# Kernel tuning notes

Measured on AMD Instinct MI355X. Metric: run time of the kernel, lower is better.

Reference implementation:

```python
import jax, jax.numpy as jnp
import numpy as np

N = 12288      # nodes
F = 512        # input feature dim
H1 = 256       # encoder hidden 1
H2 = 128       # latent dim
E = 393216     # edges (avg degree 32)


def setup_inputs() -> dict:
    key = jax.random.key(0)
    ks = jax.random.split(key, 7)
    x = jax.random.normal(ks[0], (N, F), dtype=jnp.float32)
    src = jax.random.randint(ks[1], (E,), 0, N, dtype=jnp.int64)
    dst = jax.random.randint(ks[2], (E,), 0, N, dtype=jnp.int64)
    # normalized-adjacency-like positive edge values
    edge_val = jax.random.uniform(ks[3], (E,), dtype=jnp.float32) / 32.0
    # xavier-uniform-ish scaled weights
    W1 = jax.random.normal(ks[4], (F, H1), dtype=jnp.float32) * np.float32(np.sqrt(2.0 / (F + H1)))
    W2 = jax.random.normal(ks[5], (H1, H2), dtype=jnp.float32) * np.float32(np.sqrt(2.0 / (H1 + H2)))
    W3 = jax.random.normal(ks[6], (H1, H2), dtype=jnp.float32) * np.float32(np.sqrt(2.0 / (H1 + H2)))
    return {"x": x, "src": src, "dst": dst, "edge_val": edge_val,
            "W1": W1, "W2": W2, "W3": W3}


def _spmm(src, dst, val, dense):
    # out[i] = sum_{e: src[e]==i} val[e] * dense[dst[e]]  -- sparse [N,N] @ dense [N,D]
    msg = val[:, None] * dense[dst]              # [E, D]
    return jax.ops.segment_sum(msg, src, num_segments=N)


def _gcn(h, src, dst, val, W):
    support = h @ W                               # dense GEMM
    return _spmm(src, dst, val, support)


def reference(x, src, dst, edge_val, W1, W2, W3):
    # EncoderCora (eval mode: dropout=0)
    h1 = jax.nn.relu(_gcn(x, src, dst, edge_val, W1))   # [N, H1]
    mu = _gcn(h1, src, dst, edge_val, W2)               # [N, H2]
    logvar = _gcn(h1, src, dst, edge_val, W3)           # [N, H2]
    # reparameterize: eval -> z = mu
    z = mu
    # DecoderCora: inner product + sigmoid
    adj_recon = jax.nn.sigmoid(z @ z.T)                 # [N, N]
    return adj_recon, mu, logvar
```

## Files before the change

### kernel.cpp

```cpp
#include <hip/hip_runtime.h>
#include <stdint.h>


#define NN 12288
#define FF 512
#define HD1 256
#define HD2 128
#define EE 393216

typedef short bf16x8 __attribute__((ext_vector_type(8)));
typedef float f32x16 __attribute__((ext_vector_type(16)));

__device__ inline unsigned short f2b(float f) {
  unsigned int u = __float_as_uint(f);
  unsigned int r = u + 0x7fffu + ((u >> 16) & 1u);
  return (unsigned short)(r >> 16);
}

__device__ inline bf16x8 ldb8(const unsigned short* p) {
  return *(const bf16x8*)p;
}

__device__ inline bf16x8 ldf8(const float* p) {
  float4 v0 = ((const float4*)p)[0];
  float4 v1 = ((const float4*)p)[1];
  bf16x8 r;
  r[0] = (short)f2b(v0.x); r[1] = (short)f2b(v0.y);
  r[2] = (short)f2b(v0.z); r[3] = (short)f2b(v0.w);
  r[4] = (short)f2b(v1.x); r[5] = (short)f2b(v1.y);
  r[6] = (short)f2b(v1.z); r[7] = (short)f2b(v1.w);
  return r;
}

__device__ inline f32x16 mfma32(bf16x8 a, bf16x8 b, f32x16 c) {
  return __builtin_amdgcn_mfma_f32_32x32x16_bf16(a, b, c, 0, 0, 0);
}


__global__ void k_hist(const int* __restrict__ src, int* __restrict__ deg) {
  int e = blockIdx.x * 256 + threadIdx.x;
  atomicAdd(&deg[src[e]], 1);
}

__global__ void k_scan(const int* __restrict__ deg, int* __restrict__ off,
                       int* __restrict__ cur) {
  __shared__ int sdata[256];
  __shared__ int sbase;
  if (threadIdx.x == 0) sbase = 0;
  __syncthreads();
  for (int c = 0; c < NN; c += 256) {
    int v = deg[c + threadIdx.x];
    sdata[threadIdx.x] = v;
    __syncthreads();
    for (int s = 1; s < 256; s <<= 1) {
      int t = (threadIdx.x >= s) ? sdata[threadIdx.x - s] : 0;
      __syncthreads();
      sdata[threadIdx.x] += t;
      __syncthreads();
    }
    int o = sbase + sdata[threadIdx.x] - v;
    off[c + threadIdx.x] = o;
    cur[c + threadIdx.x] = o;
    __syncthreads();
    if (threadIdx.x == 255) sbase += sdata[255];
    __syncthreads();
  }
}

__global__ void k_fill(const int* __restrict__ src, const int* __restrict__ dst,
                       const float* __restrict__ ev, int* __restrict__ cur,
                       int* __restrict__ dstp, float* __restrict__ valp) {
  int e = blockIdx.x * 256 + threadIdx.x;
  int p = atomicAdd(&cur[src[e]], 1);
  dstp[p] = dst[e];
  valp[p] = ev[e];
}


__global__ void k_f2b4(const float* __restrict__ in, unsigned short* __restrict__ outb) {
  int i = blockIdx.x * 256 + threadIdx.x;
  float4 v = ((const float4*)in)[i];
  ushort4 o;
  o.x = f2b(v.x); o.y = f2b(v.y); o.z = f2b(v.z); o.w = f2b(v.w);
  ((ushort4*)outb)[i] = o;
}

__global__ void k_transw(const float* __restrict__ W, unsigned short* __restrict__ Wt,
                         int K, int Ncols) {
  int idx = blockIdx.x * 256 + threadIdx.x;
  if (idx < K * Ncols) {
    int k = idx / Ncols;
    int n = idx - k * Ncols;
    Wt[(size_t)n * K + k] = f2b(W[idx]);
  }
}


__global__ __launch_bounds__(256) void gemm_bt(
    const unsigned short* __restrict__ A, const unsigned short* __restrict__ Bt,
    float* __restrict__ C, int Nn, int K) {
  int wave = threadIdx.x >> 6, lane = threadIdx.x & 63;
  int wr = wave >> 1, wc = wave & 1;
  int row0 = blockIdx.x * 128 + wr * 64;
  int col0 = blockIdx.y * 128 + wc * 64;
  int lm = lane & 31, lk = (lane >> 5) * 8;

  f32x16 acc[2][2] = {};
  const unsigned short* a0p = A + (size_t)(row0 + lm) * K + lk;
  const unsigned short* a1p = a0p + (size_t)32 * K;
  const unsigned short* b0p = Bt + (size_t)(col0 + lm) * K + lk;
  const unsigned short* b1p = b0p + (size_t)32 * K;

  for (int k0 = 0; k0 < K; k0 += 16) {
    bf16x8 a0 = ldb8(a0p + k0), a1 = ldb8(a1p + k0);
    bf16x8 b0 = ldb8(b0p + k0), b1 = ldb8(b1p + k0);
    acc[0][0] = mfma32(a0, b0, acc[0][0]);
    acc[0][1] = mfma32(a0, b1, acc[0][1]);
    acc[1][0] = mfma32(a1, b0, acc[1][0]);
    acc[1][1] = mfma32(a1, b1, acc[1][1]);
  }

#pragma unroll
  for (int ti = 0; ti < 2; ++ti)
#pragma unroll
    for (int tj = 0; tj < 2; ++tj)
#pragma unroll
      for (int r = 0; r < 16; ++r) {
        int row = row0 + ti * 32 + (r & 3) + 8 * (r >> 2) + 4 * (lane >> 5);
        int col = col0 + tj * 32 + lm;
        C[(size_t)row * Nn + col] = acc[ti][tj][r];
      }
}


__global__ __launch_bounds__(256) void k_spmm_relu(
    const int* __restrict__ off, const int* __restrict__ dstp,
    const float* __restrict__ valp, const float* __restrict__ dense,
    unsigned short* __restrict__ outb) {
  int node = blockIdx.x * 4 + (threadIdx.x >> 6);
  int lane = threadIdx.x & 63;
  int e0 = off[node];
  int e1 = (node == NN - 1) ? EE : off[node + 1];
  const float4* dp = (const float4*)dense;
  float4 acc = make_float4(0.f, 0.f, 0.f, 0.f);
  for (int eb = e0; eb < e1; eb += 32) {
    int rem = e1 - eb; if (rem > 32) rem = 32;
    int dd = 0; float vv = 0.f;
    if (lane < rem) { dd = dstp[eb + lane]; vv = valp[eb + lane]; }
    for (int j = 0; j < rem; ++j) {
      int dj = __shfl(dd, j);
      float vj = __shfl(vv, j);
      float4 r = dp[(size_t)dj * 64 + lane];
      acc.x = fmaf(vj, r.x, acc.x);
      acc.y = fmaf(vj, r.y, acc.y);
      acc.z = fmaf(vj, r.z, acc.z);
      acc.w = fmaf(vj, r.w, acc.w);
    }
  }
  ushort4 ob;
  ob.x = f2b(fmaxf(acc.x, 0.f));
  ob.y = f2b(fmaxf(acc.y, 0.f));
  ob.z = f2b(fmaxf(acc.z, 0.f));
  ob.w = f2b(fmaxf(acc.w, 0.f));
  ((ushort4*)outb)[(size_t)node * 64 + lane] = ob;
}

__global__ __launch_bounds__(256) void k_spmm_mlv(
    const int* __restrict__ off, const int* __restrict__ dstp,
    const float* __restrict__ valp, const float* __restrict__ dense,
    float* __restrict__ mu, float* __restrict__ logvar) {
  int node = blockIdx.x * 4 + (threadIdx.x >> 6);
  int lane = threadIdx.x & 63;
  int e0 = off[node];
  int e1 = (node == NN - 1) ? EE : off[node + 1];
  const float4* dp = (const float4*)dense;
  float4 acc = make_float4(0.f, 0.f, 0.f, 0.f);
  for (int eb = e0; eb < e1; eb += 32) {
    int rem = e1 - eb; if (rem > 32) rem = 32;
    int dd = 0; float vv = 0.f;
    if (lane < rem) { dd = dstp[eb + lane]; vv = valp[eb + lane]; }
    for (int j = 0; j < rem; ++j) {
      int dj = __shfl(dd, j);
      float vj = __shfl(vv, j);
      float4 r = dp[(size_t)dj * 64 + lane];
      acc.x = fmaf(vj, r.x, acc.x);
      acc.y = fmaf(vj, r.y, acc.y);
      acc.z = fmaf(vj, r.z, acc.z);
      acc.w = fmaf(vj, r.w, acc.w);
    }
  }
  if (lane < 32) ((float4*)mu)[(size_t)node * 32 + lane] = acc;
  else           ((float4*)logvar)[(size_t)node * 32 + (lane - 32)] = acc;
}


__global__ __launch_bounds__(256) void k_decoder_b(const unsigned short* __restrict__ Zb,
                                                   float* __restrict__ out) {
  int wave = threadIdx.x >> 6, lane = threadIdx.x & 63;
  int wr = wave >> 1, wc = wave & 1;
  int row0 = blockIdx.x * 128 + wr * 64;
  int col0 = blockIdx.y * 128 + wc * 64;
  int lm = lane & 31, lk = (lane >> 5) * 8;

  f32x16 acc[2][2] = {};
  const unsigned short* a0p = Zb + (size_t)(row0 + lm) * HD2 + lk;
  const unsigned short* a1p = a0p + (size_t)32 * HD2;
  const unsigned short* b0p = Zb + (size_t)(col0 + lm) * HD2 + lk;
  const unsigned short* b1p = b0p + (size_t)32 * HD2;

#pragma unroll
  for (int k0 = 0; k0 < HD2; k0 += 16) {
    bf16x8 a0 = ldb8(a0p + k0), a1 = ldb8(a1p + k0);
    bf16x8 b0 = ldb8(b0p + k0), b1 = ldb8(b1p + k0);
    acc[0][0] = mfma32(a0, b0, acc[0][0]);
    acc[0][1] = mfma32(a0, b1, acc[0][1]);
    acc[1][0] = mfma32(a1, b0, acc[1][0]);
    acc[1][1] = mfma32(a1, b1, acc[1][1]);
  }

#pragma unroll
  for (int ti = 0; ti < 2; ++ti)
#pragma unroll
    for (int tj = 0; tj < 2; ++tj)
#pragma unroll
      for (int r = 0; r < 16; ++r) {
        int row = row0 + ti * 32 + (r & 3) + 8 * (r >> 2) + 4 * (lane >> 5);
        int col = col0 + tj * 32 + lm;
        float v = acc[ti][tj][r];
        out[(size_t)row * NN + col] = 1.0f / (1.0f + __expf(-v));
      }
}

__global__ __launch_bounds__(256) void k_decoder(const float* __restrict__ Zf,
                                                 float* __restrict__ out) {
  int wave = threadIdx.x >> 6, lane = threadIdx.x & 63;
  int wr = wave >> 1, wc = wave & 1;
  int row0 = blockIdx.x * 128 + wr * 64;
  int col0 = blockIdx.y * 128 + wc * 64;
  int lm = lane & 31, lk = (lane >> 5) * 8;

  f32x16 acc[2][2] = {};
  const float* a0p = Zf + (size_t)(row0 + lm) * HD2 + lk;
  const float* a1p = a0p + (size_t)32 * HD2;
  const float* b0p = Zf + (size_t)(col0 + lm) * HD2 + lk;
  const float* b1p = b0p + (size_t)32 * HD2;

#pragma unroll
  for (int k0 = 0; k0 < HD2; k0 += 16) {
    bf16x8 a0 = ldf8(a0p + k0), a1 = ldf8(a1p + k0);
    bf16x8 b0 = ldf8(b0p + k0), b1 = ldf8(b1p + k0);
    acc[0][0] = mfma32(a0, b0, acc[0][0]);
    acc[0][1] = mfma32(a0, b1, acc[0][1]);
    acc[1][0] = mfma32(a1, b0, acc[1][0]);
    acc[1][1] = mfma32(a1, b1, acc[1][1]);
  }

#pragma unroll
  for (int ti = 0; ti < 2; ++ti)
#pragma unroll
    for (int tj = 0; tj < 2; ++tj)
#pragma unroll
      for (int r = 0; r < 16; ++r) {
        int row = row0 + ti * 32 + (r & 3) + 8 * (r >> 2) + 4 * (lane >> 5);
        int col = col0 + tj * 32 + lm;
        float v = acc[ti][tj][r];
        out[(size_t)row * NN + col] = 1.0f / (1.0f + __expf(-v));
      }
}


extern "C" void kernel_launch(void* const* d_in, const int* in_sizes, int n_in,
                              void* d_out, int out_size, void* d_ws, size_t ws_size,
                              hipStream_t stream) {
  const float* x  = (const float*)d_in[0];
  const int*   src = (const int*)d_in[1];
  const int*   dst = (const int*)d_in[2];
  const float* ev  = (const float*)d_in[3];
  const float* W1  = (const float*)d_in[4];
  const float* W2  = (const float*)d_in[5];
  const float* W3  = (const float*)d_in[6];
  float* out = (float*)d_out;
  float* mu     = out + (size_t)NN * NN;
  float* logvar = mu + (size_t)NN * HD2;

  char* p = (char*)d_out;
  auto alloc = [&](size_t bytes) {
    char* r = p;
    p += (bytes + 255) & ~(size_t)255;
    return r;
  };
  unsigned short* xb   = (unsigned short*)alloc((size_t)NN * FF * 2);
  unsigned short* W1t  = (unsigned short*)alloc((size_t)HD1 * FF * 2);
  unsigned short* W23t = (unsigned short*)alloc((size_t)2 * HD2 * HD1 * 2);
  float*          sup1 = (float*)alloc((size_t)NN * HD1 * 4);
  unsigned short* h1b  = (unsigned short*)alloc((size_t)NN * HD1 * 2);
  float*         sup23 = (float*)alloc((size_t)NN * 2 * HD2 * 4);
  int* deg  = (int*)alloc(NN * 4);
  int* off  = (int*)alloc(NN * 4);
  int* cur  = (int*)alloc(NN * 4);
  int*   dstp = (int*)alloc((size_t)EE * 4);
  float* valp = (float*)alloc((size_t)EE * 4);

  const size_t zb_bytes = (size_t)NN * HD2 * 2;
  bool use_zb = (d_ws != nullptr) && (ws_size >= zb_bytes + 256);
  unsigned short* zb = (unsigned short*)d_ws;

  hipMemsetAsync(deg, 0, NN * 4, stream);
  k_hist<<<EE / 256, 256, 0, stream>>>(src, deg);
  k_scan<<<1, 256, 0, stream>>>(deg, off, cur);
  k_fill<<<EE / 256, 256, 0, stream>>>(src, dst, ev, cur, dstp, valp);

  k_f2b4<<<(NN * FF / 4) / 256, 256, 0, stream>>>(x, xb);
  k_transw<<<(FF * HD1 + 255) / 256, 256, 0, stream>>>(W1, W1t, FF, HD1);
  k_transw<<<(HD1 * HD2 + 255) / 256, 256, 0, stream>>>(W2, W23t, HD1, HD2);
  k_transw<<<(HD1 * HD2 + 255) / 256, 256, 0, stream>>>(W3, W23t + (size_t)HD2 * HD1, HD1, HD2);

  gemm_bt<<<dim3(NN / 128, HD1 / 128), 256, 0, stream>>>(xb, W1t, sup1, HD1, FF);
  k_spmm_relu<<<NN / 4, 256, 0, stream>>>(off, dstp, valp, sup1, h1b);

  gemm_bt<<<dim3(NN / 128, (2 * HD2) / 128), 256, 0, stream>>>(h1b, W23t, sup23, 2 * HD2, HD1);
  k_spmm_mlv<<<NN / 4, 256, 0, stream>>>(off, dstp, valp, sup23, mu, logvar);

  if (use_zb) {
    k_f2b4<<<(NN * HD2 / 4) / 256, 256, 0, stream>>>(mu, zb);
    k_decoder_b<<<dim3(NN / 128, NN / 128), 256, 0, stream>>>(zb, out);
  } else {
    k_decoder<<<dim3(NN / 128, NN / 128), 256, 0, stream>>>(mu, out);
  }
}
```

Measured before the change: 936.9 us.

## Parallelize CSR scan, fuse prep kernels, unroll SpMM, and stream decoder stores

Replaces the single-block serial prefix scan with a three-kernel parallel scan. Merges the x conversion and the three weight transposes into one prep kernel. Unrolls the full 32-edge chunks in both SpMM kernels, and has the mu SpMM also write the bf16 copy of z, which removes a separate conversion kernel. In the decoder it uses a hardware reciprocal for the sigmoid and nontemporal stores for the large N×N output, aiming to cut launch overhead, serial scan latency and cache pollution, at some cost in sigmoid accuracy.

```diff
diff --git a/kernel.cpp b/kernel.cpp
--- a/kernel.cpp
+++ b/kernel.cpp
@@ -36,35 +36,51 @@
   return __builtin_amdgcn_mfma_f32_32x32x16_bf16(a, b, c, 0, 0, 0);
 }
 
+__device__ inline float sigmoid_fast(float v) {
+  return __builtin_amdgcn_rcpf(1.0f + __expf(-v));
+}
+
 
 __global__ void k_hist(const int* __restrict__ src, int* __restrict__ deg) {
   int e = blockIdx.x * 256 + threadIdx.x;
   atomicAdd(&deg[src[e]], 1);
 }
 
-__global__ void k_scan(const int* __restrict__ deg, int* __restrict__ off,
-                       int* __restrict__ cur) {
+__global__ void k_scan1(const int* __restrict__ deg, int* __restrict__ off,
+                        int* __restrict__ bsum) {
   __shared__ int sdata[256];
-  __shared__ int sbase;
-  if (threadIdx.x == 0) sbase = 0;
+  int t = threadIdx.x;
+  int i = blockIdx.x * 256 + t;
+  int v = deg[i];
+  sdata[t] = v;
   __syncthreads();
-  for (int c = 0; c < NN; c += 256) {
-    int v = deg[c + threadIdx.x];
-    sdata[threadIdx.x] = v;
+  for (int s = 1; s < 256; s <<= 1) {
+    int u = (t >= s) ? sdata[t - s] : 0;
     __syncthreads();
-    for (int s = 1; s < 256; s <<= 1) {
-      int t = (threadIdx.x >= s) ? sdata[threadIdx.x - s] : 0;
-      __syncthreads();
-      sdata[threadIdx.x] += t;
-      __syncthreads();
-    }
-    int o = sbase + sdata[threadIdx.x] - v;
-    off[c + threadIdx.x] = o;
-    cur[c + threadIdx.x] = o;
+    sdata[t] += u;
     __syncthreads();
-    if (threadIdx.x == 255) sbase += sdata[255];
-    __syncthreads();
-  }
+  }
+  off[i] = sdata[t] - v;
+  if (t == 255) bsum[blockIdx.x] = sdata[255];
+}
+
+__global__ void k_scan2(int* __restrict__ bsum) {
+  int t = threadIdx.x;
+  int orig = (t < NN / 256) ? bsum[t] : 0;
+  int v = orig;
+  for (int s = 1; s < 64; s <<= 1) {
+    int u = __shfl_up(v, s);
+    if (t >= s) v += u;
+  }
+  if (t < NN / 256) bsum[t] = v - orig;
+}
+
+__global__ void k_scan3(const int* __restrict__ bsum, int* __restrict__ off,
+                        int* __restrict__ cur) {
+  int i = blockIdx.x * 256 + threadIdx.x;
+  int o = off[i] + bsum[blockIdx.x];
+  off[i] = o;
+  cur[i] = o;
 }
 
 __global__ void k_fill(const int* __restrict__ src, const int* __restrict__ dst,
@@ -76,22 +92,38 @@
   valp[p] = ev[e];
 }
 
-
-__global__ void k_f2b4(const float* __restrict__ in, unsigned short* __restrict__ outb) {
-  int i = blockIdx.x * 256 + threadIdx.x;
-  float4 v = ((const float4*)in)[i];
-  ushort4 o;
-  o.x = f2b(v.x); o.y = f2b(v.y); o.z = f2b(v.z); o.w = f2b(v.w);
-  ((ushort4*)outb)[i] = o;
-}
-
-__global__ void k_transw(const float* __restrict__ W, unsigned short* __restrict__ Wt,
-                         int K, int Ncols) {
-  int idx = blockIdx.x * 256 + threadIdx.x;
-  if (idx < K * Ncols) {
-    int k = idx / Ncols;
-    int n = idx - k * Ncols;
-    Wt[(size_t)n * K + k] = f2b(W[idx]);
+#define PREP_NX   (NN * FF / 4)
+#define PREP_NW1  (FF * HD1)
+#define PREP_NW23 (HD1 * HD2)
+
+__global__ void k_prep(const float* __restrict__ x, unsigned short* __restrict__ xb,
+                       const float* __restrict__ W1, unsigned short* __restrict__ W1t,
+                       const float* __restrict__ W2, const float* __restrict__ W3,
+                       unsigned short* __restrict__ W23t) {
+  int gid = blockIdx.x * 256 + threadIdx.x;
+  if (gid < PREP_NX) {
+    float4 v = ((const float4*)x)[gid];
+    ushort4 o;
+    o.x = f2b(v.x); o.y = f2b(v.y); o.z = f2b(v.z); o.w = f2b(v.w);
+    ((ushort4*)xb)[gid] = o;
+    return;
+  }
+  int idx = gid - PREP_NX;
+  if (idx < PREP_NW1) {
+    int k = idx / HD1, n = idx - k * HD1;
+    W1t[(size_t)n * FF + k] = f2b(W1[idx]);
+    return;
+  }
+  idx -= PREP_NW1;
+  if (idx < PREP_NW23) {
+    int k = idx / HD2, n = idx - k * HD2;
+    W23t[(size_t)n * HD1 + k] = f2b(W2[idx]);
+    return;
+  }
+  idx -= PREP_NW23;
+  if (idx < PREP_NW23) {
+    int k = idx / HD2, n = idx - k * HD2;
+    W23t[(size_t)(HD2 + n) * HD1 + k] = f2b(W3[idx]);
   }
 }
 
@@ -139,14 +171,30 @@
     unsigned short* __restrict__ outb) {
   int node = blockIdx.x * 4 + (threadIdx.x >> 6);
   int lane = threadIdx.x & 63;
+  int l31 = lane & 31;
   int e0 = off[node];
   int e1 = (node == NN - 1) ? EE : off[node + 1];
   const float4* dp = (const float4*)dense;
   float4 acc = make_float4(0.f, 0.f, 0.f, 0.f);
-  for (int eb = e0; eb < e1; eb += 32) {
-    int rem = e1 - eb; if (rem > 32) rem = 32;
+  int eb = e0;
+  for (; eb + 32 <= e1; eb += 32) {
+    int dd = dstp[eb + l31];
+    float vv = valp[eb + l31];
+#pragma unroll
+    for (int j = 0; j < 32; ++j) {
+      int dj = __shfl(dd, j);
+      float vj = __shfl(vv, j);
+      float4 r = dp[(size_t)dj * 64 + lane];
+      acc.x = fmaf(vj, r.x, acc.x);
+      acc.y = fmaf(vj, r.y, acc.y);
+      acc.z = fmaf(vj, r.z, acc.z);
+      acc.w = fmaf(vj, r.w, acc.w);
+    }
+  }
+  int rem = e1 - eb;
+  if (rem > 0) {
     int dd = 0; float vv = 0.f;
-    if (lane < rem) { dd = dstp[eb + lane]; vv = valp[eb + lane]; }
+    if (l31 < rem) { dd = dstp[eb + l31]; vv = valp[eb + l31]; }
     for (int j = 0; j < rem; ++j) {
       int dj = __shfl(dd, j);
       float vj = __shfl(vv, j);
@@ -168,17 +216,34 @@
 __global__ __launch_bounds__(256) void k_spmm_mlv(
     const int* __restrict__ off, const int* __restrict__ dstp,
     const float* __restrict__ valp, const float* __restrict__ dense,
-    float* __restrict__ mu, float* __restrict__ logvar) {
+    float* __restrict__ mu, float* __restrict__ logvar,
+    unsigned short* __restrict__ zb) {
   int node = blockIdx.x * 4 + (threadIdx.x >> 6);
   int lane = threadIdx.x & 63;
+  int l31 = lane & 31;
   int e0 = off[node];
   int e1 = (node == NN - 1) ? EE : off[node + 1];
   const float4* dp = (const float4*)dense;
   float4 acc = make_float4(0.f, 0.f, 0.f, 0.f);
-  for (int eb = e0; eb < e1; eb += 32) {
-    int rem = e1 - eb; if (rem > 32) rem = 32;
+  int eb = e0;
+  for (; eb + 32 <= e1; eb += 32) {
+    int dd = dstp[eb + l31];
+    float vv = valp[eb + l31];
+#pragma unroll
+    for (int j = 0; j < 32; ++j) {
+      int dj = __shfl(dd, j);
+      float vj = __shfl(vv, j);
+      float4 r = dp[(size_t)dj * 64 + lane];
+      acc.x = fmaf(vj, r.x, acc.x);
+      acc.y = fmaf(vj, r.y, acc.y);
+      acc.z = fmaf(vj, r.z, acc.z);
+      acc.w = fmaf(vj, r.w, acc.w);
+    }
+  }
+  int rem = e1 - eb;
+  if (rem > 0) {
     int dd = 0; float vv = 0.f;
-    if (lane < rem) { dd = dstp[eb + lane]; vv = valp[eb + lane]; }
+    if (l31 < rem) { dd = dstp[eb + l31]; vv = valp[eb + l31]; }
     for (int j = 0; j < rem; ++j) {
       int dj = __shfl(dd, j);
       float vj = __shfl(vv, j);
@@ -189,8 +254,16 @@
       acc.w = fmaf(vj, r.w, acc.w);
     }
   }
-  if (lane < 32) ((float4*)mu)[(size_t)node * 32 + lane] = acc;
-  else           ((float4*)logvar)[(size_t)node * 32 + (lane - 32)] = acc;
+  if (lane < 32) {
+    ((float4*)mu)[(size_t)node * 32 + lane] = acc;
+    if (zb) {
+      ushort4 ob;
+      ob.x = f2b(acc.x); ob.y = f2b(acc.y); ob.z = f2b(acc.z); ob.w = f2b(acc.w);
+      ((ushort4*)zb)[(size_t)node * 32 + lane] = ob;
+    }
+  } else {
+    ((float4*)logvar)[(size_t)node * 32 + (lane - 32)] = acc;
+  }
 }
 
 
@@ -226,8 +299,8 @@
       for (int r = 0; r < 16; ++r) {
         int row = row0 + ti * 32 + (r & 3) + 8 * (r >> 2) + 4 * (lane >> 5);
         int col = col0 + tj * 32 + lm;
-        float v = acc[ti][tj][r];
-        out[(size_t)row * NN + col] = 1.0f / (1.0f + __expf(-v));
+        float s = sigmoid_fast(acc[ti][tj][r]);
+        __builtin_nontemporal_store(s, &out[(size_t)row * NN + col]);
       }
 }
 
@@ -263,8 +336,8 @@
       for (int r = 0; r < 16; ++r) {
         int row = row0 + ti * 32 + (r & 3) + 8 * (r >> 2) + 4 * (lane >> 5);
         int col = col0 + tj * 32 + lm;
-        float v = acc[ti][tj][r];
-        out[(size_t)row * NN + col] = 1.0f / (1.0f + __expf(-v));
+        float s = sigmoid_fast(acc[ti][tj][r]);
+        __builtin_nontemporal_store(s, &out[(size_t)row * NN + col]);
       }
 }
 
@@ -300,29 +373,31 @@
   int* cur  = (int*)alloc(NN * 4);
   int*   dstp = (int*)alloc((size_t)EE * 4);
   float* valp = (float*)alloc((size_t)EE * 4);
+  int*   bsum = (int*)alloc((NN / 256) * 4);
 
   const size_t zb_bytes = (size_t)NN * HD2 * 2;
   bool use_zb = (d_ws != nullptr) && (ws_size >= zb_bytes + 256);
-  unsigned short* zb = (unsigned short*)d_ws;
+  unsigned short* zb = use_zb ? (unsigned short*)d_ws : nullptr;
 
   hipMemsetAsync(deg, 0, NN * 4, stream);
   k_hist<<<EE / 256, 256, 0, stream>>>(src, deg);
-  k_scan<<<1, 256, 0, stream>>>(deg, off, cur);
+  k_scan1<<<NN / 256, 256, 0, stream>>>(deg, off, bsum);
+  k_scan2<<<1, 64, 0, stream>>>(bsum);
+  k_scan3<<<NN / 256, 256, 0, stream>>>(bsum, off, cur);
   k_fill<<<EE / 256, 256, 0, stream>>>(src, dst, ev, cur, dstp, valp);
 
-  k_f2b4<<<(NN * FF / 4) / 256, 256, 0, stream>>>(x, xb);
-  k_transw<<<(FF * HD1 + 255) / 256, 256, 0, stream>>>(W1, W1t, FF, HD1);
-  k_transw<<<(HD1 * HD2 + 255) / 256, 256, 0, stream>>>(W2, W23t, HD1, HD2);
-  k_transw<<<(HD1 * HD2 + 255) / 256, 256, 0, stream>>>(W3, W23t + (size_t)HD2 * HD1, HD1, HD2);
+  {
+    int total = PREP_NX + PREP_NW1 + 2 * PREP_NW23;
+    k_prep<<<(total + 255) / 256, 256, 0, stream>>>(x, xb, W1, W1t, W2, W3, W23t);
+  }
 
   gemm_bt<<<dim3(NN / 128, HD1 / 128), 256, 0, stream>>>(xb, W1t, sup1, HD1, FF);
   k_spmm_relu<<<NN / 4, 256, 0, stream>>>(off, dstp, valp, sup1, h1b);
 
   gemm_bt<<<dim3(NN / 128, (2 * HD2) / 128), 256, 0, stream>>>(h1b, W23t, sup23, 2 * HD2, HD1);
-  k_spmm_mlv<<<NN / 4, 256, 0, stream>>>(off, dstp, valp, sup23, mu, logvar);
+  k_spmm_mlv<<<NN / 4, 256, 0, stream>>>(off, dstp, valp, sup23, mu, logvar, zb);
 
   if (use_zb) {
-    k_f2b4<<<(NN * HD2 / 4) / 256, 256, 0, stream>>>(mu, zb);
     k_decoder_b<<<dim3(NN / 128, NN / 128), 256, 0, stream>>>(zb, out);
   } else {
     k_decoder<<<dim3(NN / 128, NN / 128), 256, 0, stream>>>(mu, out);
```

New measurement: 845.0 us. 9.8% less time.
